# Kernel tuning notes

Hardware: AMD Instinct MI355X
Metric: run time of the kernel (lower is better)

## Reference

```python
import jax, jax.numpy as jnp
import numpy as np

EMBED_DIM = 1024
NUM_HEADS = 16
HEAD_DIM = EMBED_DIM // NUM_HEADS
B, L = 4, 2048


def _xavier(key, out_dim, in_dim):
    limit = jnp.sqrt(6.0 / (in_dim + out_dim))
    return jax.random.uniform(key, (out_dim, in_dim), jnp.float32, -limit, limit)


def setup_inputs() -> dict:
    key = jax.random.key(0)
    kx, kq, kk, kv, ko = jax.random.split(key, 5)
    return {
        "x": jax.random.normal(kx, (B, L, EMBED_DIM), jnp.float32),
        "Wq": _xavier(kq, EMBED_DIM, EMBED_DIM), "bq": jnp.zeros((EMBED_DIM,), jnp.float32),
        "Wk": _xavier(kk, EMBED_DIM, EMBED_DIM), "bk": jnp.zeros((EMBED_DIM,), jnp.float32),
        "Wv": _xavier(kv, EMBED_DIM, EMBED_DIM), "bv": jnp.zeros((EMBED_DIM,), jnp.float32),
        "Wo": _xavier(ko, EMBED_DIM, EMBED_DIM), "bo": jnp.zeros((EMBED_DIM,), jnp.float32),
    }


def reference(x, Wq, bq, Wk, bk, Wv, bv, Wo, bo):
    bs, l, e = x.shape
    h, hd = NUM_HEADS, HEAD_DIM
    # torch Linear: y = x @ W.T + b
    q = (x @ Wq.T + bq).reshape(bs, l, h, hd).transpose(0, 2, 1, 3)  # [b,h,l,hd]
    k = (x @ Wk.T + bk).reshape(bs, l, h, hd).transpose(0, 2, 1, 3)
    v = (x @ Wv.T + bv).reshape(bs, l, h, hd).transpose(0, 2, 1, 3)
    scale = 1.0 / jnp.sqrt(jnp.asarray(hd, x.dtype))
    scores = jnp.einsum("bhqd,bhkd->bhqk", q, k) * scale  # [b,h,l,l]
    attn = jax.nn.softmax(scores, axis=-1)
    out = jnp.einsum("bhqk,bhkd->bhqd", attn, v)  # [b,h,l,hd]
    out = out.transpose(0, 2, 1, 3).reshape(bs, l, e)
    return out @ Wo.T + bo
```

## Files before the change

### kernel.cpp

```cpp
#include <hip/hip_runtime.h>
#include <stdint.h>

#define NB 4
#define NL 2048
#define NE 1024
#define NH 16
#define ND 64
#define NM (NB*NL)

typedef float f32x4 __attribute__((ext_vector_type(4)));
typedef short s16x8 __attribute__((ext_vector_type(8)));

__device__ __forceinline__ unsigned short f2b(float f) {
  uint32_t u = __float_as_uint(f);
  u += 0x7fffu + ((u >> 16) & 1u);
  return (unsigned short)(u >> 16);
}

__device__ __forceinline__ uint32_t pk2(float a, float b) {
  return (uint32_t)f2b(a) | ((uint32_t)f2b(b) << 16);
}

__device__ __forceinline__ void gload16(const void* g, void* l) {
  __builtin_amdgcn_global_load_lds((const __attribute__((address_space(1))) void*)g,
                                   (__attribute__((address_space(3))) void*)l, 16, 0, 0);
}

__global__ void cvt_kernel(const float* __restrict__ in, unsigned short* __restrict__ out, int n8) {
  int stride = gridDim.x * blockDim.x;
  for (int i = blockIdx.x * blockDim.x + threadIdx.x; i < n8; i += stride) {
    const float4* p = (const float4*)in + (size_t)i * 2;
    float4 a = p[0], b = p[1];
    s16x8 r;
    r[0] = (short)f2b(a.x); r[1] = (short)f2b(a.y); r[2] = (short)f2b(a.z); r[3] = (short)f2b(a.w);
    r[4] = (short)f2b(b.x); r[5] = (short)f2b(b.y); r[6] = (short)f2b(b.z); r[7] = (short)f2b(b.w);
    *((s16x8*)out + i) = r;
  }
}

__global__ void cvt4_kernel(const float* __restrict__ w0, const float* __restrict__ w1,
                            const float* __restrict__ w2, const float* __restrict__ w3,
                            unsigned short* __restrict__ o0, unsigned short* __restrict__ o1,
                            unsigned short* __restrict__ o2, unsigned short* __restrict__ o3,
                            int n8) {
  const int y = blockIdx.y;
  const float* in = (y == 0) ? w0 : (y == 1) ? w1 : (y == 2) ? w2 : w3;
  unsigned short* out = (y == 0) ? o0 : (y == 1) ? o1 : (y == 2) ? o2 : o3;
  int stride = gridDim.x * blockDim.x;
  for (int i = blockIdx.x * blockDim.x + threadIdx.x; i < n8; i += stride) {
    const float4* p = (const float4*)in + (size_t)i * 2;
    float4 a = p[0], b = p[1];
    s16x8 r;
    r[0] = (short)f2b(a.x); r[1] = (short)f2b(a.y); r[2] = (short)f2b(a.z); r[3] = (short)f2b(a.w);
    r[4] = (short)f2b(b.x); r[5] = (short)f2b(b.y); r[6] = (short)f2b(b.z); r[7] = (short)f2b(b.w);
    *((s16x8*)out + i) = r;
  }
}

template<int MODE>
__launch_bounds__(256, 3)
__global__ void gemm_bt(const unsigned short* __restrict__ A,
                        const unsigned short* __restrict__ W0,
                        const unsigned short* __restrict__ W1,
                        const unsigned short* __restrict__ W2,
                        const float* __restrict__ b0,
                        const float* __restrict__ b1,
                        const float* __restrict__ b2,
                        unsigned short* __restrict__ O0,
                        unsigned short* __restrict__ O1,
                        unsigned short* __restrict__ O2,
                        float* __restrict__ fout)
{
  __shared__ alignas(16) char smem[32768];
  char* sA = smem;
  char* sB = smem + 16384;

  const int tid = threadIdx.x;
  const int lane = tid & 63;
  const int wid = tid >> 6;
  const int bx = blockIdx.x, by = blockIdx.y;
  const int m0 = by * 128;

  int which = 0;
  const unsigned short* Wsel;
  const float* bias;
  int n0;
  if (MODE == 0) {
    which = bx >> 3;
    Wsel = (which == 0) ? W0 : ((which == 1) ? W1 : W2);
    bias = (which == 0) ? b0 : ((which == 1) ? b1 : b2);
    n0 = (bx & 7) * 128;
  } else {
    Wsel = W0; bias = b0; n0 = bx * 128;
  }

  const int wr = (wid >> 1) * 64;
  const int wc = (wid & 1) * 64;
  int aaddr[4], baddr[4];
#pragma unroll
  for (int m = 0; m < 4; ++m) {
    int ra = wr + m * 16 + (lane & 15);
    aaddr[m] = ra * 128 + (((lane >> 4) * 16) ^ ((ra & 7) << 4));
    int rb = wc + m * 16 + (lane & 15);
    baddr[m] = rb * 128 + (((lane >> 4) * 16) ^ ((rb & 7) << 4));
  }

  f32x4 acc[4][4] = {};
  const int c0 = wid * 64 + lane;

  for (int kt = 0; kt < 16; ++kt) {
    const int k0 = kt * 64;
#pragma unroll
    for (int it = 0; it < 4; ++it) {
      int c = it * 256 + c0;
      int row = c >> 3;
      int sb = ((((c & 7) << 4)) ^ ((row & 7) << 4)) >> 1;
      gload16(A    + (size_t)(m0 + row) * NE + k0 + sb, sA + it * 4096 + wid * 1024);
      gload16(Wsel + (size_t)(n0 + row) * NE + k0 + sb, sB + it * 4096 + wid * 1024);
    }
    __syncthreads();
#pragma unroll
    for (int kk = 0; kk < 2; ++kk) {
      s16x8 af[4], bf[4];
#pragma unroll
      for (int m = 0; m < 4; ++m) af[m] = *(const s16x8*)(sA + (aaddr[m] ^ (kk << 6)));
#pragma unroll
      for (int n = 0; n < 4; ++n) bf[n] = *(const s16x8*)(sB + (baddr[n] ^ (kk << 6)));
#pragma unroll
      for (int m = 0; m < 4; ++m)
#pragma unroll
        for (int n = 0; n < 4; ++n)
          acc[m][n] = __builtin_amdgcn_mfma_f32_16x16x32_bf16(af[m], bf[n], acc[m][n], 0, 0, 0);
    }
    __syncthreads();
  }

  const float qsc = (MODE == 0 && ((bx >> 3) == 0)) ? 0.18033688011112042f : 1.0f;
#pragma unroll
  for (int m = 0; m < 4; ++m) {
    const int row0 = m0 + wr + m * 16 + ((lane >> 4) << 2);
#pragma unroll
    for (int n = 0; n < 4; ++n) {
      const int col = n0 + wc + n * 16 + (lane & 15);
      const float bv = bias[col];
      if (MODE == 1) {
#pragma unroll
        for (int r = 0; r < 4; ++r)
          fout[(size_t)(row0 + r) * NE + col] = acc[m][n][r] + bv;
      } else {
        const int b = row0 >> 11;
        const int l = row0 & 2047;
        const int h = col >> 6;
        const int d = col & 63;
        if (which < 2) {
          unsigned short* dst = (which == 0) ? O0 : O1;
#pragma unroll
          for (int r = 0; r < 4; ++r)
            dst[((size_t)(b * NH + h) * NL + (l + r)) * ND + d] = f2b((acc[m][n][r] + bv) * qsc);
        } else {
          ushort4 pk;
          pk.x = f2b(acc[m][n][0] + bv);
          pk.y = f2b(acc[m][n][1] + bv);
          pk.z = f2b(acc[m][n][2] + bv);
          pk.w = f2b(acc[m][n][3] + bv);
          *(ushort4*)(O2 + ((size_t)(b * NH + h) * ND + d) * NL + l) = pk;
        }
      }
    }
  }
}

__launch_bounds__(256, 3)
__global__ void attn_kernel(const unsigned short* __restrict__ Q,
                            const unsigned short* __restrict__ K,
                            const unsigned short* __restrict__ Vt,
                            unsigned short* __restrict__ AO)
{
  __shared__ alignas(16) char smem[49152];

  const int tid = threadIdx.x;
  const int lane = tid & 63;
  const int wid = tid >> 6;
  const int hi = lane >> 4;
  const int qi = lane & 15;
  const int qt = blockIdx.x;
  const int bh = blockIdx.y;
  const int b = bh >> 4;
  const int h = bh & 15;
  const size_t base = (size_t)bh * NL * ND;
  const int q0 = qt * 128 + wid * 32;

  s16x8 qf[2][2];
#pragma unroll
  for (int m = 0; m < 2; ++m)
#pragma unroll
    for (int kk = 0; kk < 2; ++kk)
      qf[m][kk] = *(const s16x8*)(Q + base + (size_t)(q0 + m * 16 + qi) * ND
                                  + kk * 32 + hi * 8);

  f32x4 o[2][4] = {};
  float rm[2] = {-1e30f, -1e30f};
  float rl[2] = {0.f, 0.f};

  int kaddr[4], vaddr[4];
#pragma unroll
  for (int n = 0; n < 4; ++n) {
    int rk = n * 16 + qi;
    kaddr[n] = rk * 128 + ((hi * 16) ^ ((rk & 7) << 4));
    vaddr[n] = kaddr[n];
  }
  char* sP = smem + 32768 + wid * 4096;
  int pwoff[4], proff[2];
#pragma unroll
  for (int n = 0; n < 4; ++n)
    pwoff[n] = qi * 128 + ((n * 32 + hi * 8) ^ ((qi & 7) << 4));
#pragma unroll
  for (int ks = 0; ks < 2; ++ks)
    proff[ks] = qi * 128 + ((ks * 64 + hi * 16) ^ ((qi & 7) << 4));

#define STAGE(T, BUF)                                                          \
  do {                                                                         \
    const int kv0_ = (T) * 64;                                                 \
    char* sKb_ = smem + (BUF) * 8192;                                          \
    char* sVb_ = smem + 16384 + (BUF) * 8192;                                  \
    _Pragma("unroll")                                                          \
    for (int it = 0; it < 2; ++it) {                                           \
      int c = it * 256 + wid * 64 + lane;                                      \
      int row = c >> 3;                                                        \
      int sb = (((c & 7) << 4) ^ ((row & 7) << 4)) >> 1;                       \
      gload16(K  + base + (size_t)(kv0_ + row) * ND + sb,                      \
              sKb_ + it * 4096 + wid * 1024);                                  \
      gload16(Vt + base + (size_t)row * NL + kv0_ + sb,                        \
              sVb_ + it * 4096 + wid * 1024);                                  \
    }                                                                          \
  } while (0)

  STAGE(0, 0);
  __syncthreads();

  for (int t = 0; t < 32; ++t) {
    const int cur = t & 1;
    if (t < 31) STAGE(t + 1, cur ^ 1);
    const char* sKb = smem + cur * 8192;
    const char* sVb = smem + 16384 + cur * 8192;

    f32x4 s[2][4] = {};
#pragma unroll
    for (int kk = 0; kk < 2; ++kk) {
      s16x8 kf[4];
#pragma unroll
      for (int n = 0; n < 4; ++n) kf[n] = *(const s16x8*)(sKb + (kaddr[n] ^ (kk << 6)));
#pragma unroll
      for (int m = 0; m < 2; ++m)
#pragma unroll
        for (int n = 0; n < 4; ++n)
          s[m][n] = __builtin_amdgcn_mfma_f32_16x16x32_bf16(kf[n], qf[m][kk], s[m][n], 0, 0, 0);
    }

#pragma unroll
    for (int m = 0; m < 2; ++m) {
      float pm = s[m][0][0];
#pragma unroll
      for (int n = 0; n < 4; ++n)
#pragma unroll
        for (int r = 0; r < 4; ++r) pm = fmaxf(pm, s[m][n][r]);
      pm = fmaxf(pm, __shfl_xor(pm, 16));
      pm = fmaxf(pm, __shfl_xor(pm, 32));
      float mn = rm[m];
      if (!__all(pm - mn <= 8.0f)) {
        mn = fmaxf(mn, pm);
        float al = __builtin_amdgcn_exp2f(rm[m] - mn);
        rl[m] *= al;
#pragma unroll
        for (int dt = 0; dt < 4; ++dt) o[m][dt] = o[m][dt] * al;
        rm[m] = mn;
      }
      float ts = 0.f;
#pragma unroll
      for (int n = 0; n < 4; ++n) {
        float p0 = __builtin_amdgcn_exp2f(s[m][n][0] - mn);
        float p1 = __builtin_amdgcn_exp2f(s[m][n][1] - mn);
        float p2 = __builtin_amdgcn_exp2f(s[m][n][2] - mn);
        float p3 = __builtin_amdgcn_exp2f(s[m][n][3] - mn);
        ts += (p0 + p1) + (p2 + p3);
        uint2 w;
        w.x = pk2(p0, p1);
        w.y = pk2(p2, p3);
        *(uint2*)(sP + m * 2048 + pwoff[n]) = w;
      }
      ts += __shfl_xor(ts, 16);
      ts += __shfl_xor(ts, 32);
      rl[m] += ts;
    }

#pragma unroll
    for (int ks = 0; ks < 2; ++ks) {
      s16x8 vf[4];
#pragma unroll
      for (int dt = 0; dt < 4; ++dt) vf[dt] = *(const s16x8*)(sVb + (vaddr[dt] ^ (ks << 6)));
#pragma unroll
      for (int m = 0; m < 2; ++m) {
        s16x8 pf = *(const s16x8*)(sP + m * 2048 + proff[ks]);
#pragma unroll
        for (int dt = 0; dt < 4; ++dt)
          o[m][dt] = __builtin_amdgcn_mfma_f32_16x16x32_bf16(vf[dt], pf, o[m][dt], 0, 0, 0);
      }
    }
    __syncthreads();
  }
#undef STAGE

#pragma unroll
  for (int m = 0; m < 2; ++m) {
    const float inv = 1.0f / rl[m];
    const int qg = q0 + m * 16 + qi;
#pragma unroll
    for (int dt = 0; dt < 4; ++dt) {
      ushort4 pk;
      pk.x = f2b(o[m][dt][0] * inv);
      pk.y = f2b(o[m][dt][1] * inv);
      pk.z = f2b(o[m][dt][2] * inv);
      pk.w = f2b(o[m][dt][3] * inv);
      *(ushort4*)(AO + (size_t)(b * NL + qg) * NE + h * 64 + dt * 16 + hi * 4) = pk;
    }
  }
}

extern "C" void kernel_launch(void* const* d_in, const int* in_sizes, int n_in,
                              void* d_out, int out_size, void* d_ws, size_t ws_size,
                              hipStream_t stream) {
  const float* x  = (const float*)d_in[0];
  const float* Wq = (const float*)d_in[1];
  const float* bq = (const float*)d_in[2];
  const float* Wk = (const float*)d_in[3];
  const float* bk = (const float*)d_in[4];
  const float* Wv = (const float*)d_in[5];
  const float* bv = (const float*)d_in[6];
  const float* Wo = (const float*)d_in[7];
  const float* bo = (const float*)d_in[8];
  float* out = (float*)d_out;
  char* ws = (char*)d_ws;

  unsigned short* xb  = (unsigned short*)(ws);
  unsigned short* AOw = (unsigned short*)(ws);
  unsigned short* wqb = (unsigned short*)(ws + (16u << 20));
  unsigned short* wkb = (unsigned short*)(ws + (18u << 20));
  unsigned short* wvb = (unsigned short*)(ws + (20u << 20));
  unsigned short* wob = (unsigned short*)(ws + (22u << 20));
  unsigned short* Qw  = (unsigned short*)(ws + (24u << 20));
  unsigned short* Kw  = (unsigned short*)(ws + (40u << 20));
  unsigned short* Vtw = (unsigned short*)(ws + (56u << 20));
  (void)in_sizes; (void)n_in; (void)out_size; (void)ws_size;

  cvt_kernel<<<1024, 256, 0, stream>>>(x, xb, (NM * NE) / 8);
  cvt4_kernel<<<dim3(128, 4), 256, 0, stream>>>(Wq, Wk, Wv, Wo,
                                                wqb, wkb, wvb, wob, (NE * NE) / 8);

  gemm_bt<0><<<dim3(24, 64), 256, 0, stream>>>(xb, wqb, wkb, wvb, bq, bk, bv,
                                               Qw, Kw, Vtw, nullptr);
  attn_kernel<<<dim3(16, 64), 256, 0, stream>>>(Qw, Kw, Vtw, AOw);
  gemm_bt<1><<<dim3(8, 64), 256, 0, stream>>>(AOw, wob, nullptr, nullptr, bo,
                                              nullptr, nullptr,
                                              nullptr, nullptr, nullptr, out);
}
```

Measured before the change: 313.6 us.

## Use packed bf16 conversion, MFMA priority hints, tree max, and lower GEMM occupancy

Replaces the manual bit-twiddling float-to-bf16 packing with the HIP __float22bfloat162_rn intrinsic, which can lower to a packed hardware convert on gfx950. It also wraps the attention MFMA blocks in s_setprio raises, turns the row-max reduction into a tree, and relaxes the GEMM launch bound from 3 to 2 waves per SIMD. The aim is fewer ALU instructions in the softmax and epilogues, better MFMA issue under contention, and more registers for the GEMM, at the cost of possibly lower GEMM occupancy.

```diff
diff --git a/kernel.cpp b/kernel.cpp
--- a/kernel.cpp
+++ b/kernel.cpp
@@ -1,4 +1,5 @@
 #include <hip/hip_runtime.h>
+#include <hip/hip_bf16.h>
 #include <stdint.h>
 
 #define NB 4
@@ -18,7 +19,8 @@
 }
 
 __device__ __forceinline__ uint32_t pk2(float a, float b) {
-  return (uint32_t)f2b(a) | ((uint32_t)f2b(b) << 16);
+  __hip_bfloat162 h = __float22bfloat162_rn(make_float2(a, b));
+  union { __hip_bfloat162 h; uint32_t u; } c; c.h = h; return c.u;
 }
 
 __device__ __forceinline__ void gload16(const void* g, void* l) {
@@ -31,10 +33,10 @@
   for (int i = blockIdx.x * blockDim.x + threadIdx.x; i < n8; i += stride) {
     const float4* p = (const float4*)in + (size_t)i * 2;
     float4 a = p[0], b = p[1];
-    s16x8 r;
-    r[0] = (short)f2b(a.x); r[1] = (short)f2b(a.y); r[2] = (short)f2b(a.z); r[3] = (short)f2b(a.w);
-    r[4] = (short)f2b(b.x); r[5] = (short)f2b(b.y); r[6] = (short)f2b(b.z); r[7] = (short)f2b(b.w);
-    *((s16x8*)out + i) = r;
+    uint4 r;
+    r.x = pk2(a.x, a.y); r.y = pk2(a.z, a.w);
+    r.z = pk2(b.x, b.y); r.w = pk2(b.z, b.w);
+    *((uint4*)out + i) = r;
   }
 }
 
@@ -50,15 +52,15 @@
   for (int i = blockIdx.x * blockDim.x + threadIdx.x; i < n8; i += stride) {
     const float4* p = (const float4*)in + (size_t)i * 2;
     float4 a = p[0], b = p[1];
-    s16x8 r;
-    r[0] = (short)f2b(a.x); r[1] = (short)f2b(a.y); r[2] = (short)f2b(a.z); r[3] = (short)f2b(a.w);
-    r[4] = (short)f2b(b.x); r[5] = (short)f2b(b.y); r[6] = (short)f2b(b.z); r[7] = (short)f2b(b.w);
-    *((s16x8*)out + i) = r;
+    uint4 r;
+    r.x = pk2(a.x, a.y); r.y = pk2(a.z, a.w);
+    r.z = pk2(b.x, b.y); r.w = pk2(b.z, b.w);
+    *((uint4*)out + i) = r;
   }
 }
 
 template<int MODE>
-__launch_bounds__(256, 3)
+__launch_bounds__(256, 2)
 __global__ void gemm_bt(const unsigned short* __restrict__ A,
                         const unsigned short* __restrict__ W0,
                         const unsigned short* __restrict__ W1,
@@ -158,12 +160,10 @@
           for (int r = 0; r < 4; ++r)
             dst[((size_t)(b * NH + h) * NL + (l + r)) * ND + d] = f2b((acc[m][n][r] + bv) * qsc);
         } else {
-          ushort4 pk;
-          pk.x = f2b(acc[m][n][0] + bv);
-          pk.y = f2b(acc[m][n][1] + bv);
-          pk.z = f2b(acc[m][n][2] + bv);
-          pk.w = f2b(acc[m][n][3] + bv);
-          *(ushort4*)(O2 + ((size_t)(b * NH + h) * ND + d) * NL + l) = pk;
+          uint2 w;
+          w.x = pk2(acc[m][n][0] + bv, acc[m][n][1] + bv);
+          w.y = pk2(acc[m][n][2] + bv, acc[m][n][3] + bv);
+          *(uint2*)(O2 + ((size_t)(b * NH + h) * ND + d) * NL + l) = w;
         }
       }
     }
@@ -245,6 +245,7 @@
     const char* sVb = smem + 16384 + cur * 8192;
 
     f32x4 s[2][4] = {};
+    __builtin_amdgcn_s_setprio(1);
 #pragma unroll
     for (int kk = 0; kk < 2; ++kk) {
       s16x8 kf[4];
@@ -256,14 +257,15 @@
         for (int n = 0; n < 4; ++n)
           s[m][n] = __builtin_amdgcn_mfma_f32_16x16x32_bf16(kf[n], qf[m][kk], s[m][n], 0, 0, 0);
     }
+    __builtin_amdgcn_s_setprio(0);
 
 #pragma unroll
     for (int m = 0; m < 2; ++m) {
-      float pm = s[m][0][0];
-#pragma unroll
-      for (int n = 0; n < 4; ++n)
-#pragma unroll
-        for (int r = 0; r < 4; ++r) pm = fmaxf(pm, s[m][n][r]);
+      float a0 = fmaxf(fmaxf(fmaxf(s[m][0][0], s[m][0][1]), s[m][0][2]), s[m][0][3]);
+      float a1 = fmaxf(fmaxf(fmaxf(s[m][1][0], s[m][1][1]), s[m][1][2]), s[m][1][3]);
+      float a2 = fmaxf(fmaxf(fmaxf(s[m][2][0], s[m][2][1]), s[m][2][2]), s[m][2][3]);
+      float a3 = fmaxf(fmaxf(fmaxf(s[m][3][0], s[m][3][1]), s[m][3][2]), s[m][3][3]);
+      float pm = fmaxf(fmaxf(a0, a1), fmaxf(a2, a3));
       pm = fmaxf(pm, __shfl_xor(pm, 16));
       pm = fmaxf(pm, __shfl_xor(pm, 32));
       float mn = rm[m];
@@ -293,6 +295,7 @@
       rl[m] += ts;
     }
 
+    __builtin_amdgcn_s_setprio(1);
 #pragma unroll
     for (int ks = 0; ks < 2; ++ks) {
       s16x8 vf[4];
@@ -306,6 +309,7 @@
           o[m][dt] = __builtin_amdgcn_mfma_f32_16x16x32_bf16(vf[dt], pf, o[m][dt], 0, 0, 0);
       }
     }
+    __builtin_amdgcn_s_setprio(0);
     __syncthreads();
   }
 #undef STAGE
@@ -316,12 +320,10 @@
     const int qg = q0 + m * 16 + qi;
 #pragma unroll
     for (int dt = 0; dt < 4; ++dt) {
-      ushort4 pk;
-      pk.x = f2b(o[m][dt][0] * inv);
-      pk.y = f2b(o[m][dt][1] * inv);
-      pk.z = f2b(o[m][dt][2] * inv);
-      pk.w = f2b(o[m][dt][3] * inv);
-      *(ushort4*)(AO + (size_t)(b * NL + qg) * NE + h * 64 + dt * 16 + hi * 4) = pk;
+      uint2 w;
+      w.x = pk2(o[m][dt][0] * inv, o[m][dt][1] * inv);
+      w.y = pk2(o[m][dt][2] * inv, o[m][dt][3] * inv);
+      *(uint2*)(AO + (size_t)(b * NL + qg) * NE + h * 64 + dt * 16 + hi * 4) = w;
     }
   }
 }
```

After: 299.4 us. 4.5% less time.
